# Optimization experiments

Hardware: AMD Instinct MI355X
Metric: run time of the kernel (lower is better)

## Reference

```python
import jax, jax.numpy as jnp
import numpy as np

N, E, F_IN, F_E = 50000, 400000, 16, 3
H1, H2, H3 = 32, 64, 64
NUM_GRAPHS = 32
SLOPE = 0.2  # GAT leaky_relu negative slope


def _glorot(key, shape):
    fan_in, fan_out = shape[0], shape[-1]
    lim = jnp.sqrt(6.0 / (fan_in + fan_out))
    return jax.random.uniform(key, shape, jnp.float32, -lim, lim)


def setup_inputs() -> dict:
    key = jax.random.key(0)
    ks = jax.random.split(key, 20)
    x = jax.random.normal(ks[0], (N, F_IN), jnp.float32)
    edge_attr = jax.random.normal(ks[1], (E, F_E), jnp.float32)
    edge_index = jax.random.randint(ks[2], (2, E), 0, N, jnp.int32)
    batch = jnp.sort(jax.random.randint(ks[3], (N,), 0, NUM_GRAPHS, jnp.int32))
    return {
        "x": x, "edge_attr": edge_attr, "edge_index": edge_index, "batch": batch,
        # EdgeMLP: F_E -> 128 -> 64 -> F_IN*H1
        "mlp_w1": _glorot(ks[4], (F_E, 128)), "mlp_b1": jnp.zeros((128,), jnp.float32),
        "mlp_w2": _glorot(ks[5], (128, 64)), "mlp_b2": jnp.zeros((64,), jnp.float32),
        "mlp_w3": _glorot(ks[6], (64, F_IN * H1)), "mlp_b3": jnp.zeros((F_IN * H1,), jnp.float32),
        # NNConv root weight + bias
        "root_w": _glorot(ks[7], (F_IN, H1)), "conv1_b": jnp.zeros((H1,), jnp.float32),
        # GATConv 1 (heads=1, concat=False)
        "gat1_w": _glorot(ks[8], (H1, H2)), "gat1_asrc": _glorot(ks[9], (H2,)),
        "gat1_adst": _glorot(ks[10], (H2,)), "gat1_b": jnp.zeros((H2,), jnp.float32),
        # GATConv 2
        "gat2_w": _glorot(ks[11], (H2, H3)), "gat2_asrc": _glorot(ks[12], (H3,)),
        "gat2_adst": _glorot(ks[13], (H3,)), "gat2_b": jnp.zeros((H3,), jnp.float32),
    }


def _segment_softmax(logits, seg, num):
    m = jax.ops.segment_max(logits, seg, num_segments=num)
    e = jnp.exp(logits - m[seg])
    s = jax.ops.segment_sum(e, seg, num_segments=num)
    return e / s[seg]


def _gat(h_in, src, dst, W, a_src, a_dst, b):
    # self loops (PyG default add_self_loops=True)
    n = h_in.shape[0]
    loop = jnp.arange(n, dtype=src.dtype)
    s = jnp.concatenate([src, loop])
    d = jnp.concatenate([dst, loop])
    h = h_in @ W  # [N, out]
    alpha = (h @ a_src)[s] + (h @ a_dst)[d]  # [E+N]
    alpha = jnp.where(alpha > 0, alpha, SLOPE * alpha)
    alpha = _segment_softmax(alpha, d, n)
    out = jax.ops.segment_sum(alpha[:, None] * h[s], d, num_segments=n)
    return out + b


def reference(x, edge_attr, edge_index, batch,
              mlp_w1, mlp_b1, mlp_w2, mlp_b2, mlp_w3, mlp_b3,
              root_w, conv1_b,
              gat1_w, gat1_asrc, gat1_adst, gat1_b,
              gat2_w, gat2_asrc, gat2_adst, gat2_b):
    src, dst = edge_index[0], edge_index[1]
    # --- NNConv: per-edge weight matrix from EdgeMLP, message = x_src @ W_e ---
    h = jax.nn.relu(edge_attr @ mlp_w1 + mlp_b1)
    h = jax.nn.relu(h @ mlp_w2 + mlp_b2)
    w_e = (h @ mlp_w3 + mlp_b3).reshape(-1, F_IN, H1)  # [E, F_IN, H1]
    msg = jnp.einsum('ei,eio->eo', x[src], w_e)        # [E, H1]
    agg = jax.ops.segment_sum(msg, dst, num_segments=N)  # aggr='add'
    h1 = jax.nn.relu(x @ root_w + agg + conv1_b)
    # --- GAT layers ---
    h2 = jax.nn.relu(_gat(h1, src, dst, gat1_w, gat1_asrc, gat1_adst, gat1_b))
    h3 = jax.nn.relu(_gat(h2, src, dst, gat2_w, gat2_asrc, gat2_adst, gat2_b))
    # --- global mean pool ---
    sums = jax.ops.segment_sum(h3, batch, num_segments=NUM_GRAPHS)
    cnt = jax.ops.segment_sum(jnp.ones((N,), h3.dtype), batch, num_segments=NUM_GRAPHS)
    return sums / jnp.maximum(cnt, 1.0)[:, None]
```

## Files before the change

kernel.cpp:

```cpp
#include <hip/hip_runtime.h>

#define NN 50000
#define NE 400000
#define NG 32
#define SLOPE 0.2f
#define NSB ((NN + 255) / 256)

typedef __attribute__((ext_vector_type(4))) float f32x4;
typedef __attribute__((ext_vector_type(16))) float f32x16;
typedef __attribute__((ext_vector_type(8))) short s16x8;

__device__ __forceinline__ float lrelu(float v) { return v > 0.f ? v : SLOPE * v; }
__device__ __forceinline__ unsigned short f2bf(float f) {
    union { float f; unsigned u; } c; c.f = f;
    unsigned r = c.u + 0x7fffu + ((c.u >> 16) & 1u);
    return (unsigned short)(r >> 16);
}
__device__ __forceinline__ float bf2f(unsigned short b) {
    union { unsigned u; float f; } c; c.u = ((unsigned)b) << 16; return c.f;
}
__device__ __forceinline__ unsigned pack2(float a, float b) {
    return (unsigned)f2bf(a) | ((unsigned)f2bf(b) << 16);
}
__device__ __forceinline__ uint2 pack_bf4(float a, float b, float c, float d) {
    uint2 u;
    u.x = pack2(a, b);
    u.y = pack2(c, d);
    return u;
}

__global__ __launch_bounds__(256) void k_hist(const int* __restrict__ dst, int* __restrict__ deg) {
    int e = blockIdx.x * 256 + threadIdx.x;
    if (e < NE) atomicAdd(&deg[dst[e]], 1);
}

__global__ __launch_bounds__(256) void k_bsum(const int* __restrict__ deg, int* __restrict__ bsum) {
    __shared__ int ls[256];
    const int t = threadIdx.x;
    const int idx = blockIdx.x * 256 + t;
    ls[t] = (idx < NN) ? deg[idx] : 0;
    __syncthreads();
#pragma unroll
    for (int off = 128; off; off >>= 1) {
        if (t < off) ls[t] += ls[t + off];
        __syncthreads();
    }
    if (t == 0) bsum[blockIdx.x] = ls[0];
}

__global__ __launch_bounds__(256) void k_scan2(const int* __restrict__ deg,
                                               const int* __restrict__ bsum,
                                               int* __restrict__ rowptr, int* __restrict__ cursor) {
    __shared__ int lb[256];
    __shared__ int ls[256];
    const int t = threadIdx.x, b = blockIdx.x;
    lb[t] = (t < NSB && t < b) ? bsum[t] : 0;
    const int idx = b * 256 + t;
    const int v = (idx < NN) ? deg[idx] : 0;
    ls[t] = v;
    __syncthreads();
#pragma unroll
    for (int off = 128; off; off >>= 1) {
        if (t < off) lb[t] += lb[t + off];
        __syncthreads();
    }
#pragma unroll
    for (int off = 1; off < 256; off <<= 1) {
        int u = (t >= off) ? ls[t - off] : 0;
        __syncthreads();
        ls[t] += u;
        __syncthreads();
    }
    if (idx < NN) {
        const int run = lb[0] + ls[t] - v;
        rowptr[idx] = run;
        cursor[idx] = run;
    }
    if (b == 0 && t == 0) rowptr[NN] = NE;
}

__global__ __launch_bounds__(256) void k_perm(const int* __restrict__ dst, const int* __restrict__ src,
                                              int* __restrict__ cursor, int* __restrict__ eid,
                                              int* __restrict__ srcp) {
    int e = blockIdx.x * 256 + threadIdx.x;
    if (e < NE) {
        int p = atomicAdd(&cursor[dst[e]], 1);
        eid[p] = e;
        srcp[p] = src[e];
    }
}

__global__ __launch_bounds__(256) void k_wprep(const float* __restrict__ w3,
                                               const float* __restrict__ w2,
                                               const float* __restrict__ w1,
                                               const float* __restrict__ b1,
                                               const float* __restrict__ b3,
                                               unsigned short* __restrict__ w3t_g,
                                               unsigned short* __restrict__ w2t_g,
                                               unsigned short* __restrict__ w1p_g,
                                               unsigned short* __restrict__ b3t_g) {
    const int v = blockIdx.x * 256 + threadIdx.x;
    if (v < 64 * 512) {
        const int k = v >> 9, n = v & 511;
        const int byte = (n << 7) | ((k << 1) ^ ((n & 7) << 4));
        *(unsigned short*)((char*)w3t_g + byte) = f2bf(w3[v]);
    }
    if (v < 64 * 128) {
        const int o = v & 63, slot = v >> 6;
        const int ks = slot >> 4, lg2 = (slot >> 3) & 1, j = slot & 7;
        const int kp = (ks >> 1) * 32 + (j & 3) + 8 * (j >> 2) + 16 * (ks & 1) + 4 * lg2;
        const int byte = (o << 8) | ((slot << 1) ^ ((o & 7) << 4));
        *(unsigned short*)((char*)w2t_g + byte) = f2bf(w2[kp * 64 + o]);
    }
    if (v < 128 * 16) {
        const int j = v >> 4, k = v & 15;
        float val = (k < 3) ? w1[k * 128 + j] : (k == 3 ? b1[j] : 0.f);
        w1p_g[v] = f2bf(val);
    }
    if (v < 512) {
        const int i = v >> 5, o = v & 31;
        b3t_g[o * 16 + i] = f2bf(b3[v]);
    }
}

#define FUSED_GRID 256
#define NCHUNK (NE / 32)
__global__ __launch_bounds__(512, 1) void k_fused(
    const float* __restrict__ ea,
    const unsigned short* __restrict__ w1p_g,
    const unsigned short* __restrict__ w2t_g, const float* __restrict__ b2,
    const unsigned short* __restrict__ w3t_g, const unsigned short* __restrict__ b3t_g,
    const int* __restrict__ src, const float* __restrict__ x,
    unsigned short* __restrict__ msg)
{
    __shared__ __align__(16) unsigned short w3t[512 * 64];
    __shared__ __align__(16) unsigned short w2t[64 * 128];
    __shared__ __align__(16) unsigned short w1p[128 * 16];
    __shared__ __align__(16) unsigned short b3t[512];
    __shared__ __align__(16) float b2s[64];
    __shared__ __align__(16) unsigned slab[8][1024];

    const int t = threadIdx.x;
    {
        const uint4* g = (const uint4*)w3t_g;
        uint4* l = (uint4*)w3t;
        for (int v = t; v < 4096; v += 512) l[v] = g[v];
        const uint4* g2 = (const uint4*)w2t_g;
        uint4* l2 = (uint4*)w2t;
        for (int v = t; v < 1024; v += 512) l2[v] = g2[v];
    }
    if (t < 256) ((uint4*)w1p)[t] = ((const uint4*)w1p_g)[t];
    if (t < 64)  ((uint4*)b3t)[t] = ((const uint4*)b3t_g)[t];
    if (t < 64)  b2s[t] = b2[t];
    __syncthreads();

    const int wid = t >> 6, lane = t & 63;
    const int l31 = lane & 31, lg2 = lane >> 5;
    char* sw = (char*)slab[wid];
    const int swz = (l31 & 7) << 4;

    s16x8 w1pf[4];
#pragma unroll
    for (int n = 0; n < 4; ++n)
        w1pf[n] = *(const s16x8*)((const char*)w1p + ((n * 32 + l31) << 5) + lg2 * 16);
    s16x8 b3f = *(const s16x8*)((const char*)b3t + (l31 << 5) + lg2 * 16);

    for (int chunk = blockIdx.x * 8 + wid; chunk < NCHUNK; chunk += FUSED_GRID * 8) {
        const int e = chunk * 32 + l31;
        const int sn = src[e];
        const f32x4* __restrict__ xp = (const f32x4*)(x + (size_t)sn * 16);
        f32x4 x0 = xp[0], x1 = xp[1], x2 = xp[2], x3 = xp[3];
        const float ea0 = ea[e * 3], ea1 = ea[e * 3 + 1], ea2 = ea[e * 3 + 2];

        s16x8 eb = (s16x8){0, 0, 0, 0, 0, 0, 0, 0};
        if (lg2 == 0) {
            eb[0] = (short)f2bf(ea0); eb[1] = (short)f2bf(ea1);
            eb[2] = (short)f2bf(ea2); eb[3] = (short)0x3F80;
        }
        s16x8 hb[8];
#pragma unroll
        for (int n = 0; n < 4; ++n) {
            f32x16 d = {0.f};
            d = __builtin_amdgcn_mfma_f32_32x32x16_bf16(w1pf[n], eb, d, 0, 0, 0);
#pragma unroll
            for (int s = 0; s < 2; ++s)
#pragma unroll
                for (int j = 0; j < 8; ++j)
                    hb[2 * n + s][j] = (short)f2bf(fmaxf(d[(j & 3) + 4 * (j >> 2) + 8 * s], 0.f));
        }

        asm volatile("s_waitcnt lgkmcnt(0)" ::: "memory");
#pragma unroll
        for (int nblk = 0; nblk < 2; ++nblk) {
            f32x16 a2 = {0.f};
            const char* __restrict__ w2row = (const char*)w2t + ((nblk * 32 + l31) << 8);
#pragma unroll
            for (int ks = 0; ks < 8; ++ks) {
                s16x8 a = *(const s16x8*)(w2row + ((ks * 32 + lg2 * 16) ^ swz));
                a2 = __builtin_amdgcn_mfma_f32_32x32x16_bf16(a, hb[ks], a2, 0, 0, 0);
            }
#pragma unroll
            for (int rh = 0; rh < 4; ++rh) {
                const f32x4 bv = *(const f32x4*)(b2s + nblk * 32 + rh * 8 + lg2 * 4);
                const int kb = nblk * 64 + rh * 16 + lg2 * 8;
                *(uint2*)(sw + l31 * 128 + (kb ^ swz)) =
                    pack_bf4(fmaxf(a2[rh * 4] + bv[0], 0.f), fmaxf(a2[rh * 4 + 1] + bv[1], 0.f),
                             fmaxf(a2[rh * 4 + 2] + bv[2], 0.f), fmaxf(a2[rh * 4 + 3] + bv[3], 0.f));
            }
        }
        asm volatile("s_waitcnt lgkmcnt(0)" ::: "memory");

        s16x8 wb[4];
#pragma unroll
        for (int ks = 0; ks < 4; ++ks)
            wb[ks] = *(const s16x8*)(sw + l31 * 128 + ((ks * 32 + lg2 * 16) ^ swz));

        s16x8 xbf;
        {
            f32x4 a0 = lg2 ? x2 : x0, a1 = lg2 ? x3 : x1;
#pragma unroll
            for (int i = 0; i < 4; ++i) {
                xbf[i] = (short)f2bf(a0[i]);
                xbf[i + 4] = (short)f2bf(a1[i]);
            }
        }
        f32x16 p = {0.f};
        p = __builtin_amdgcn_mfma_f32_32x32x16_bf16(b3f, xbf, p, 0, 0, 0);

#pragma unroll
        for (int nblk = 0; nblk < 16; ++nblk) {
            const char* __restrict__ arow = (const char*)w3t + ((nblk * 32 + l31) << 7);
            f32x16 d = {0.f};
#pragma unroll
            for (int ks = 0; ks < 4; ++ks) {
                s16x8 a = *(const s16x8*)(arow + ((ks * 32 + lg2 * 16) ^ swz));
                d = __builtin_amdgcn_mfma_f32_32x32x16_bf16(a, wb[ks], d, 0, 0, 0);
            }
            const float xs = (nblk < 4 ? x0 : nblk < 8 ? x1 : nblk < 12 ? x2 : x3)[nblk & 3];
#pragma unroll
            for (int r = 0; r < 16; ++r) p[r] = fmaf(xs, d[r], p[r]);
        }

        asm volatile("s_waitcnt lgkmcnt(0)" ::: "memory");
#pragma unroll
        for (int rh = 0; rh < 4; ++rh) {
            const int ob = rh * 16 + lg2 * 8;
            *(uint2*)(sw + l31 * 64 + (ob ^ ((l31 & 7) << 3))) =
                pack_bf4(p[rh * 4], p[rh * 4 + 1], p[rh * 4 + 2], p[rh * 4 + 3]);
        }
        asm volatile("s_waitcnt lgkmcnt(0)" ::: "memory");
#pragma unroll
        for (int q = 0; q < 2; ++q) {
            const int er = (lane >> 2) + q * 16;
            const int off = (lane & 3) * 16;
            const int s8 = (er & 7) << 3;
            uint2 a = *(const uint2*)(sw + er * 64 + (off ^ s8));
            uint2 b = *(const uint2*)(sw + er * 64 + ((off + 8) ^ s8));
            *(uint4*)((char*)msg + (size_t)chunk * 2048 + q * 1024 + lane * 16) =
                make_uint4(a.x, a.y, b.x, b.y);
        }
    }
}

__global__ __launch_bounds__(256) void k_agg(
    const unsigned short* __restrict__ msg, const int* __restrict__ rowptr,
    const int* __restrict__ eid, const float* __restrict__ x,
    const float* __restrict__ rw, const float* __restrict__ cb, float* __restrict__ h1)
{
    const int gid = blockIdx.x * 256 + threadIdx.x;
    const int n = (gid >> 6) * 2 + ((gid & 63) >> 5);
    if (n >= NN) return;
    const int o = gid & 31;
    const int r0 = rowptr[n], r1 = rowptr[n + 1];
    float acc = 0.f;
    for (int j = r0; j < r1; ++j)
        acc += bf2f(msg[(size_t)eid[j] * 32 + o]);
    const float* __restrict__ xr = x + (size_t)n * 16;
    float root = cb[o];
#pragma unroll
    for (int i = 0; i < 16; ++i) root = fmaf(xr[i], rw[i * 32 + o], root);
    h1[(size_t)n * 32 + o] = fmaxf(acc + root, 0.f);
}

template <int FI, bool BFIN>
__global__ __launch_bounds__(256) void k_gat_h(
    const void* __restrict__ hin, const float* __restrict__ W,
    const float* __restrict__ av_s, const float* __restrict__ av_d,
    unsigned* __restrict__ hbf, float* __restrict__ as_v, float* __restrict__ ad_v)
{
    const int n = blockIdx.x * 256 + threadIdx.x;
    if (n >= NN) return;
    float acc[64];
#pragma unroll
    for (int o = 0; o < 64; ++o) acc[o] = 0.f;

    float xv[FI];
    if constexpr (BFIN) {
        const uint4* __restrict__ hp = (const uint4*)((const unsigned*)hin + (size_t)n * (FI / 2));
#pragma unroll
        for (int q = 0; q < FI / 8; ++q) {
            uint4 v = hp[q];
            const unsigned w4[4] = {v.x, v.y, v.z, v.w};
#pragma unroll
            for (int c = 0; c < 4; ++c) {
                xv[q * 8 + 2 * c]     = bf2f((unsigned short)(w4[c] & 0xffff));
                xv[q * 8 + 2 * c + 1] = bf2f((unsigned short)(w4[c] >> 16));
            }
        }
    } else {
        const f32x4* __restrict__ hp = (const f32x4*)((const float*)hin + (size_t)n * FI);
#pragma unroll
        for (int q = 0; q < FI / 4; ++q) {
            f32x4 v = hp[q];
#pragma unroll
            for (int c = 0; c < 4; ++c) xv[q * 4 + c] = v[c];
        }
    }
#pragma unroll 2
    for (int i = 0; i < FI; ++i) {
        const float xi = xv[i];
        const float* __restrict__ wr = W + i * 64;
#pragma unroll
        for (int o = 0; o < 64; ++o) acc[o] = fmaf(xi, wr[o], acc[o]);
    }
    float s = 0.f, d = 0.f;
#pragma unroll
    for (int o = 0; o < 64; ++o) {
        s = fmaf(acc[o], av_s[o], s);
        d = fmaf(acc[o], av_d[o], d);
    }
    as_v[n] = s;
    ad_v[n] = d;
    uint4* __restrict__ op = (uint4*)(hbf + (size_t)n * 32);
#pragma unroll
    for (int q = 0; q < 8; ++q)
        op[q] = make_uint4(pack2(acc[8 * q], acc[8 * q + 1]), pack2(acc[8 * q + 2], acc[8 * q + 3]),
                           pack2(acc[8 * q + 4], acc[8 * q + 5]), pack2(acc[8 * q + 6], acc[8 * q + 7]));
}

__global__ __launch_bounds__(256) void k_easrc(const int* __restrict__ srcp,
                                               const float* __restrict__ as_v,
                                               float* __restrict__ asp) {
    int j = blockIdx.x * 256 + threadIdx.x;
    if (j < NE) asp[j] = as_v[srcp[j]];
}

__global__ __launch_bounds__(256) void k_gat_node(
    const int* __restrict__ rowptr, const int* __restrict__ srcp, const float* __restrict__ asp,
    const unsigned* __restrict__ hbf, const float* __restrict__ as_v, const float* __restrict__ ad_v,
    const float* __restrict__ b, unsigned* __restrict__ outbf)
{
    const int n = (blockIdx.x * 256 + threadIdx.x) >> 6;
    if (n >= NN) return;
    const int lane = threadIdx.x & 63;
    const int fl = lane & 15, qw = lane >> 4;
    const int r0 = rowptr[n], r1 = rowptr[n + 1];
    const float adn = ad_v[n];
    const float l_self = lrelu(as_v[n] + adn);
    float m = l_self;
    for (int j = r0 + lane; j < r1; j += 64)
        m = fmaxf(m, lrelu(asp[j] + adn));
#pragma unroll
    for (int off = 32; off; off >>= 1) m = fmaxf(m, __shfl_xor(m, off));
    float s = 0.f;
    for (int j = r0 + lane; j < r1; j += 64)
        s += expf(lrelu(asp[j] + adn) - m);
#pragma unroll
    for (int off = 32; off; off >>= 1) s += __shfl_xor(s, off);
    const float w_self = expf(l_self - m);
    s += w_self;
    float a0 = 0.f, a1 = 0.f, a2 = 0.f, a3 = 0.f;
    if (qw == 0) {
        const uint2 hv = *(const uint2*)(hbf + (size_t)n * 32 + fl * 2);
        a0 = w_self * bf2f((unsigned short)(hv.x & 0xffff));
        a1 = w_self * bf2f((unsigned short)(hv.x >> 16));
        a2 = w_self * bf2f((unsigned short)(hv.y & 0xffff));
        a3 = w_self * bf2f((unsigned short)(hv.y >> 16));
    }
    for (int j = r0 + qw; j < r1; j += 4) {
        const int sn = srcp[j];
        const float w = expf(lrelu(asp[j] + adn) - m);
        const uint2 hv = *(const uint2*)(hbf + (size_t)sn * 32 + fl * 2);
        a0 = fmaf(w, bf2f((unsigned short)(hv.x & 0xffff)), a0);
        a1 = fmaf(w, bf2f((unsigned short)(hv.x >> 16)), a1);
        a2 = fmaf(w, bf2f((unsigned short)(hv.y & 0xffff)), a2);
        a3 = fmaf(w, bf2f((unsigned short)(hv.y >> 16)), a3);
    }
#pragma unroll
    for (int off = 16; off <= 32; off <<= 1) {
        a0 += __shfl_xor(a0, off);
        a1 += __shfl_xor(a1, off);
        a2 += __shfl_xor(a2, off);
        a3 += __shfl_xor(a3, off);
    }
    if (qw == 0) {
        const float v0 = fmaxf(a0 / s + b[4 * fl], 0.f);
        const float v1 = fmaxf(a1 / s + b[4 * fl + 1], 0.f);
        const float v2 = fmaxf(a2 / s + b[4 * fl + 2], 0.f);
        const float v3 = fmaxf(a3 / s + b[4 * fl + 3], 0.f);
        *(uint2*)(outbf + (size_t)n * 32 + fl * 2) = make_uint2(pack2(v0, v1), pack2(v2, v3));
    }
}

__global__ __launch_bounds__(256) void k_pool1(
    const unsigned* __restrict__ hbf, const int* __restrict__ batch,
    float* __restrict__ gsum, float* __restrict__ gcnt)
{
    __shared__ float ls[NG * 64];
    __shared__ float lc[NG];
    for (int j = threadIdx.x; j < NG * 64; j += 256) ls[j] = 0.f;
    if (threadIdx.x < NG) lc[threadIdx.x] = 0.f;
    __syncthreads();
    const int base = blockIdx.x * 512;
    for (int idx = threadIdx.x; idx < 512 * 32; idx += 256) {
        const int nl = idx >> 5, f2 = idx & 31;
        const int n = base + nl;
        if (n < NN) {
            const int g = batch[n];
            const unsigned hv = hbf[(size_t)n * 32 + f2];
            atomicAdd(&ls[g * 64 + 2 * f2], bf2f((unsigned short)(hv & 0xffff)));
            atomicAdd(&ls[g * 64 + 2 * f2 + 1], bf2f((unsigned short)(hv >> 16)));
            if (f2 == 0) atomicAdd(&lc[g], 1.f);
        }
    }
    __syncthreads();
    for (int j = threadIdx.x; j < NG * 64; j += 256) atomicAdd(&gsum[j], ls[j]);
    if (threadIdx.x < NG) atomicAdd(&gcnt[threadIdx.x], lc[threadIdx.x]);
}

__global__ __launch_bounds__(256) void k_pool2(
    const float* __restrict__ gsum, const float* __restrict__ gcnt, float* __restrict__ out)
{
    const int idx = blockIdx.x * 256 + threadIdx.x;
    if (idx >= NG * 64) return;
    out[idx] = gsum[idx] / fmaxf(gcnt[idx >> 6], 1.f);
}

extern "C" void kernel_launch(void* const* d_in, const int* in_sizes, int n_in,
                              void* d_out, int out_size, void* d_ws, size_t ws_size,
                              hipStream_t stream)
{
    const float* x     = (const float*)d_in[0];
    const float* ea    = (const float*)d_in[1];
    const int*   ei    = (const int*)d_in[2];
    const int*   batch = (const int*)d_in[3];
    const float* w1 = (const float*)d_in[4];   const float* b1 = (const float*)d_in[5];
    const float* w2 = (const float*)d_in[6];   const float* b2 = (const float*)d_in[7];
    const float* w3 = (const float*)d_in[8];   const float* b3 = (const float*)d_in[9];
    const float* rw = (const float*)d_in[10];  const float* cb = (const float*)d_in[11];
    const float* g1w  = (const float*)d_in[12]; const float* g1as = (const float*)d_in[13];
    const float* g1ad = (const float*)d_in[14]; const float* g1b  = (const float*)d_in[15];
    const float* g2w  = (const float*)d_in[16]; const float* g2as = (const float*)d_in[17];
    const float* g2ad = (const float*)d_in[18]; const float* g2b  = (const float*)d_in[19];
    const int* src = ei;
    const int* dst = ei + NE;
    float* out = (float*)d_out;
    (void)in_sizes; (void)n_in; (void)out_size; (void)ws_size;

    char* ws = (char*)d_ws;
    size_t off = 0;
    auto alloc = [&](size_t bytes) -> char* {
        char* p = ws + off;
        off += (bytes + 255) & ~(size_t)255;
        return p;
    };
    int*  deg    = (int*)alloc((size_t)NN * 4);
    int*  cursor = (int*)alloc((size_t)NN * 4);
    int*  rowptr = (int*)alloc((size_t)(NN + 1) * 4);
    int*  bsum   = (int*)alloc((size_t)NSB * 4);
    int*  eid    = (int*)alloc((size_t)NE * 4);
    int*  srcp   = (int*)alloc((size_t)NE * 4);
    float* asp   = (float*)alloc((size_t)NE * 4);
    unsigned short* w3t_g = (unsigned short*)alloc((size_t)64 * 512 * 2);
    unsigned short* w2t_g = (unsigned short*)alloc((size_t)64 * 128 * 2);
    unsigned short* w1p_g = (unsigned short*)alloc((size_t)128 * 16 * 2);
    unsigned short* b3t_g = (unsigned short*)alloc((size_t)512 * 2);
    unsigned short* msg   = (unsigned short*)alloc((size_t)NE * 32 * 2);
    float* h1    = (float*)alloc((size_t)NN * 32 * 4);
    unsigned* hT = (unsigned*)alloc((size_t)NN * 32 * 4);
    unsigned* hC = (unsigned*)alloc((size_t)NN * 32 * 4);
    unsigned* hD = (unsigned*)alloc((size_t)NN * 32 * 4);
    float* as_v = (float*)alloc((size_t)NN * 4);
    float* ad_v = (float*)alloc((size_t)NN * 4);
    float* gsum = (float*)alloc((size_t)NG * 64 * 4);
    float* gcnt = (float*)alloc((size_t)NG * 4);

    hipMemsetAsync(deg, 0, (size_t)NN * 4, stream);
    hipMemsetAsync(gsum, 0, (size_t)NG * 64 * 4, stream);
    hipMemsetAsync(gcnt, 0, (size_t)NG * 4, stream);

    k_hist<<<(NE + 255) / 256, 256, 0, stream>>>(dst, deg);
    k_bsum<<<NSB, 256, 0, stream>>>(deg, bsum);
    k_scan2<<<NSB, 256, 0, stream>>>(deg, bsum, rowptr, cursor);
    k_perm<<<(NE + 255) / 256, 256, 0, stream>>>(dst, src, cursor, eid, srcp);

    k_wprep<<<(64 * 512 + 255) / 256, 256, 0, stream>>>(w3, w2, w1, b1, b3,
                                                        w3t_g, w2t_g, w1p_g, b3t_g);
    k_fused<<<FUSED_GRID, 512, 0, stream>>>(ea, w1p_g, w2t_g, b2, w3t_g, b3t_g, src, x, msg);
    k_agg<<<(NN / 2 * 64 + 255) / 256 + 1, 256, 0, stream>>>(msg, rowptr, eid, x, rw, cb, h1);

    k_gat_h<32, false><<<(NN + 255) / 256, 256, 0, stream>>>(h1, g1w, g1as, g1ad, hT, as_v, ad_v);
    k_easrc<<<(NE + 255) / 256, 256, 0, stream>>>(srcp, as_v, asp);
    k_gat_node<<<(NN * 64 + 255) / 256, 256, 0, stream>>>(rowptr, srcp, asp, hT, as_v, ad_v, g1b, hC);

    k_gat_h<64, true><<<(NN + 255) / 256, 256, 0, stream>>>(hC, g2w, g2as, g2ad, hT, as_v, ad_v);
    k_easrc<<<(NE + 255) / 256, 256, 0, stream>>>(srcp, as_v, asp);
    k_gat_node<<<(NN * 64 + 255) / 256, 256, 0, stream>>>(rowptr, srcp, asp, hT, as_v, ad_v, g2b, hD);

    k_pool1<<<(NN + 511) / 512, 256, 0, stream>>>(hD, batch, gsum, gcnt);
    k_pool2<<<(NG * 64 + 255) / 256, 256, 0, stream>>>(gsum, gcnt, out);
}
```

Measured before the change: 334.4 us.

## Fuse GAT feature transforms into aggregation kernels and double fused-MLP block size

Folds the per-node GAT linear transform and attention-score projections into the preceding aggregation kernels (NNConv aggregation feeds GAT1 transform; GAT1 node softmax feeds GAT2 transform), computing each row with one wavefront using shuffles. This removes the separate k_gat_h launches and the h1/hC intermediate round trips through global memory. It also raises the fused edge-MLP kernel from 512 to 1024 threads per block, with 16 waves and a doubled LDS slab, which increases LDS use and register pressure per block. The cost is more shuffle traffic per node and repeated reads of W rows per wavefront.

```diff
diff --git a/kernel.cpp b/kernel.cpp
--- a/kernel.cpp
+++ b/kernel.cpp
@@ -125,7 +125,7 @@
 
 #define FUSED_GRID 256
 #define NCHUNK (NE / 32)
-__global__ __launch_bounds__(512, 1) void k_fused(
+__global__ __launch_bounds__(1024) void k_fused(
     const float* __restrict__ ea,
     const unsigned short* __restrict__ w1p_g,
     const unsigned short* __restrict__ w2t_g, const float* __restrict__ b2,
@@ -138,16 +138,16 @@
     __shared__ __align__(16) unsigned short w1p[128 * 16];
     __shared__ __align__(16) unsigned short b3t[512];
     __shared__ __align__(16) float b2s[64];
-    __shared__ __align__(16) unsigned slab[8][1024];
+    __shared__ __align__(16) unsigned slab[16][1024];
 
     const int t = threadIdx.x;
     {
         const uint4* g = (const uint4*)w3t_g;
         uint4* l = (uint4*)w3t;
-        for (int v = t; v < 4096; v += 512) l[v] = g[v];
+        for (int v = t; v < 4096; v += 1024) l[v] = g[v];
         const uint4* g2 = (const uint4*)w2t_g;
         uint4* l2 = (uint4*)w2t;
-        for (int v = t; v < 1024; v += 512) l2[v] = g2[v];
+        if (t < 1024) { if (t < 1024) l2[t % 1024] = g2[t % 1024]; }
     }
     if (t < 256) ((uint4*)w1p)[t] = ((const uint4*)w1p_g)[t];
     if (t < 64)  ((uint4*)b3t)[t] = ((const uint4*)b3t_g)[t];
@@ -165,7 +165,7 @@
         w1pf[n] = *(const s16x8*)((const char*)w1p + ((n * 32 + l31) << 5) + lg2 * 16);
     s16x8 b3f = *(const s16x8*)((const char*)b3t + (l31 << 5) + lg2 * 16);
 
-    for (int chunk = blockIdx.x * 8 + wid; chunk < NCHUNK; chunk += FUSED_GRID * 8) {
+    for (int chunk = blockIdx.x * 16 + wid; chunk < NCHUNK; chunk += FUSED_GRID * 16) {
         const int e = chunk * 32 + l31;
         const int sn = src[e];
         const f32x4* __restrict__ xp = (const f32x4*)(x + (size_t)sn * 16);
@@ -262,80 +262,37 @@
     }
 }
 
-__global__ __launch_bounds__(256) void k_agg(
+__global__ __launch_bounds__(256) void k_aggt(
     const unsigned short* __restrict__ msg, const int* __restrict__ rowptr,
     const int* __restrict__ eid, const float* __restrict__ x,
-    const float* __restrict__ rw, const float* __restrict__ cb, float* __restrict__ h1)
-{
-    const int gid = blockIdx.x * 256 + threadIdx.x;
-    const int n = (gid >> 6) * 2 + ((gid & 63) >> 5);
+    const float* __restrict__ rw, const float* __restrict__ cb,
+    const float* __restrict__ W, const float* __restrict__ av_s, const float* __restrict__ av_d,
+    unsigned* __restrict__ hbf, float* __restrict__ as_v, float* __restrict__ ad_v)
+{
+    const int n = (blockIdx.x * 256 + threadIdx.x) >> 6;
     if (n >= NN) return;
-    const int o = gid & 31;
+    const int lane = threadIdx.x & 63;
+    const int half = lane >> 5, o = lane & 31;
     const int r0 = rowptr[n], r1 = rowptr[n + 1];
-    float acc = 0.f;
-    for (int j = r0; j < r1; ++j)
-        acc += bf2f(msg[(size_t)eid[j] * 32 + o]);
+    float agg = 0.f;
+    for (int j = r0 + half; j < r1; j += 2)
+        agg += bf2f(msg[(size_t)eid[j] * 32 + o]);
+    agg += __shfl_xor(agg, 32);
     const float* __restrict__ xr = x + (size_t)n * 16;
     float root = cb[o];
 #pragma unroll
     for (int i = 0; i < 16; ++i) root = fmaf(xr[i], rw[i * 32 + o], root);
-    h1[(size_t)n * 32 + o] = fmaxf(acc + root, 0.f);
-}
-
-template <int FI, bool BFIN>
-__global__ __launch_bounds__(256) void k_gat_h(
-    const void* __restrict__ hin, const float* __restrict__ W,
-    const float* __restrict__ av_s, const float* __restrict__ av_d,
-    unsigned* __restrict__ hbf, float* __restrict__ as_v, float* __restrict__ ad_v)
-{
-    const int n = blockIdx.x * 256 + threadIdx.x;
-    if (n >= NN) return;
-    float acc[64];
-#pragma unroll
-    for (int o = 0; o < 64; ++o) acc[o] = 0.f;
-
-    float xv[FI];
-    if constexpr (BFIN) {
-        const uint4* __restrict__ hp = (const uint4*)((const unsigned*)hin + (size_t)n * (FI / 2));
-#pragma unroll
-        for (int q = 0; q < FI / 8; ++q) {
-            uint4 v = hp[q];
-            const unsigned w4[4] = {v.x, v.y, v.z, v.w};
-#pragma unroll
-            for (int c = 0; c < 4; ++c) {
-                xv[q * 8 + 2 * c]     = bf2f((unsigned short)(w4[c] & 0xffff));
-                xv[q * 8 + 2 * c + 1] = bf2f((unsigned short)(w4[c] >> 16));
-            }
-        }
-    } else {
-        const f32x4* __restrict__ hp = (const f32x4*)((const float*)hin + (size_t)n * FI);
-#pragma unroll
-        for (int q = 0; q < FI / 4; ++q) {
-            f32x4 v = hp[q];
-#pragma unroll
-            for (int c = 0; c < 4; ++c) xv[q * 4 + c] = v[c];
-        }
-    }
-#pragma unroll 2
-    for (int i = 0; i < FI; ++i) {
-        const float xi = xv[i];
-        const float* __restrict__ wr = W + i * 64;
-#pragma unroll
-        for (int o = 0; o < 64; ++o) acc[o] = fmaf(xi, wr[o], acc[o]);
-    }
-    float s = 0.f, d = 0.f;
-#pragma unroll
-    for (int o = 0; o < 64; ++o) {
-        s = fmaf(acc[o], av_s[o], s);
-        d = fmaf(acc[o], av_d[o], d);
-    }
-    as_v[n] = s;
-    ad_v[n] = d;
-    uint4* __restrict__ op = (uint4*)(hbf + (size_t)n * 32);
-#pragma unroll
-    for (int q = 0; q < 8; ++q)
-        op[q] = make_uint4(pack2(acc[8 * q], acc[8 * q + 1]), pack2(acc[8 * q + 2], acc[8 * q + 3]),
-                           pack2(acc[8 * q + 4], acc[8 * q + 5]), pack2(acc[8 * q + 6], acc[8 * q + 7]));
+    const float h1v = fmaxf(agg + root, 0.f);
+    float acc = 0.f;
+#pragma unroll 8
+    for (int i = 0; i < 32; ++i)
+        acc = fmaf(__shfl(h1v, i), W[i * 64 + lane], acc);
+    float s = acc * av_s[lane], d = acc * av_d[lane];
+#pragma unroll
+    for (int off = 32; off; off >>= 1) { s += __shfl_xor(s, off); d += __shfl_xor(d, off); }
+    if (lane == 0) { as_v[n] = s; ad_v[n] = d; }
+    const float nb = __shfl(acc, lane | 1);
+    if (!(lane & 1)) hbf[(size_t)n * 32 + (lane >> 1)] = pack2(acc, nb);
 }
 
 __global__ __launch_bounds__(256) void k_easrc(const int* __restrict__ srcp,
@@ -345,7 +302,79 @@
     if (j < NE) asp[j] = as_v[srcp[j]];
 }
 
-__global__ __launch_bounds__(256) void k_gat_node(
+__global__ __launch_bounds__(256) void k_gat1(
+    const int* __restrict__ rowptr, const int* __restrict__ srcp, const float* __restrict__ asp,
+    const unsigned* __restrict__ hbf, const float* __restrict__ as_v, const float* __restrict__ ad_v,
+    const float* __restrict__ b,
+    const float* __restrict__ W2, const float* __restrict__ av_s2, const float* __restrict__ av_d2,
+    unsigned* __restrict__ hbf2, float* __restrict__ as_v2, float* __restrict__ ad_v2)
+{
+    const int n = (blockIdx.x * 256 + threadIdx.x) >> 6;
+    if (n >= NN) return;
+    const int lane = threadIdx.x & 63;
+    const int fl = lane & 15, qw = lane >> 4;
+    const int r0 = rowptr[n], r1 = rowptr[n + 1];
+    const float adn = ad_v[n];
+    const float l_self = lrelu(as_v[n] + adn);
+    float m = l_self;
+    for (int j = r0 + lane; j < r1; j += 64)
+        m = fmaxf(m, lrelu(asp[j] + adn));
+#pragma unroll
+    for (int off = 32; off; off >>= 1) m = fmaxf(m, __shfl_xor(m, off));
+    float s = 0.f;
+    for (int j = r0 + lane; j < r1; j += 64)
+        s += expf(lrelu(asp[j] + adn) - m);
+#pragma unroll
+    for (int off = 32; off; off >>= 1) s += __shfl_xor(s, off);
+    const float w_self = expf(l_self - m);
+    s += w_self;
+    float a0 = 0.f, a1 = 0.f, a2 = 0.f, a3 = 0.f;
+    if (qw == 0) {
+        const uint2 hv = *(const uint2*)(hbf + (size_t)n * 32 + fl * 2);
+        a0 = w_self * bf2f((unsigned short)(hv.x & 0xffff));
+        a1 = w_self * bf2f((unsigned short)(hv.x >> 16));
+        a2 = w_self * bf2f((unsigned short)(hv.y & 0xffff));
+        a3 = w_self * bf2f((unsigned short)(hv.y >> 16));
+    }
+    for (int j = r0 + qw; j < r1; j += 4) {
+        const int sn = srcp[j];
+        const float w = expf(lrelu(asp[j] + adn) - m);
+        const uint2 hv = *(const uint2*)(hbf + (size_t)sn * 32 + fl * 2);
+        a0 = fmaf(w, bf2f((unsigned short)(hv.x & 0xffff)), a0);
+        a1 = fmaf(w, bf2f((unsigned short)(hv.x >> 16)), a1);
+        a2 = fmaf(w, bf2f((unsigned short)(hv.y & 0xffff)), a2);
+        a3 = fmaf(w, bf2f((unsigned short)(hv.y >> 16)), a3);
+    }
+#pragma unroll
+    for (int off = 16; off <= 32; off <<= 1) {
+        a0 += __shfl_xor(a0, off);
+        a1 += __shfl_xor(a1, off);
+        a2 += __shfl_xor(a2, off);
+        a3 += __shfl_xor(a3, off);
+    }
+    const float v0 = fmaxf(a0 / s + b[4 * fl], 0.f);
+    const float v1 = fmaxf(a1 / s + b[4 * fl + 1], 0.f);
+    const float v2 = fmaxf(a2 / s + b[4 * fl + 2], 0.f);
+    const float v3 = fmaxf(a3 / s + b[4 * fl + 3], 0.f);
+    float acc = 0.f;
+#pragma unroll 8
+    for (int i = 0; i < 64; ++i) {
+        float hi;
+        if ((i & 3) == 0) hi = __shfl(v0, i >> 2);
+        else if ((i & 3) == 1) hi = __shfl(v1, i >> 2);
+        else if ((i & 3) == 2) hi = __shfl(v2, i >> 2);
+        else hi = __shfl(v3, i >> 2);
+        acc = fmaf(hi, W2[i * 64 + lane], acc);
+    }
+    float s2 = acc * av_s2[lane], d2 = acc * av_d2[lane];
+#pragma unroll
+    for (int off = 32; off; off >>= 1) { s2 += __shfl_xor(s2, off); d2 += __shfl_xor(d2, off); }
+    if (lane == 0) { as_v2[n] = s2; ad_v2[n] = d2; }
+    const float nb = __shfl(acc, lane | 1);
+    if (!(lane & 1)) hbf2[(size_t)n * 32 + (lane >> 1)] = pack2(acc, nb);
+}
+
+__global__ __launch_bounds__(256) void k_gat2(
     const int* __restrict__ rowptr, const int* __restrict__ srcp, const float* __restrict__ asp,
     const unsigned* __restrict__ hbf, const float* __restrict__ as_v, const float* __restrict__ ad_v,
     const float* __restrict__ b, unsigned* __restrict__ outbf)
@@ -476,12 +505,13 @@
     unsigned short* w1p_g = (unsigned short*)alloc((size_t)128 * 16 * 2);
     unsigned short* b3t_g = (unsigned short*)alloc((size_t)512 * 2);
     unsigned short* msg   = (unsigned short*)alloc((size_t)NE * 32 * 2);
-    float* h1    = (float*)alloc((size_t)NN * 32 * 4);
-    unsigned* hT = (unsigned*)alloc((size_t)NN * 32 * 4);
-    unsigned* hC = (unsigned*)alloc((size_t)NN * 32 * 4);
-    unsigned* hD = (unsigned*)alloc((size_t)NN * 32 * 4);
-    float* as_v = (float*)alloc((size_t)NN * 4);
-    float* ad_v = (float*)alloc((size_t)NN * 4);
+    unsigned* hT  = (unsigned*)alloc((size_t)NN * 32 * 4);
+    unsigned* hT2 = (unsigned*)alloc((size_t)NN * 32 * 4);
+    unsigned* hD  = (unsigned*)alloc((size_t)NN * 32 * 4);
+    float* as_v  = (float*)alloc((size_t)NN * 4);
+    float* ad_v  = (float*)alloc((size_t)NN * 4);
+    float* as_v2 = (float*)alloc((size_t)NN * 4);
+    float* ad_v2 = (float*)alloc((size_t)NN * 4);
     float* gsum = (float*)alloc((size_t)NG * 64 * 4);
     float* gcnt = (float*)alloc((size_t)NG * 4);
 
@@ -496,16 +526,15 @@
 
     k_wprep<<<(64 * 512 + 255) / 256, 256, 0, stream>>>(w3, w2, w1, b1, b3,
                                                         w3t_g, w2t_g, w1p_g, b3t_g);
-    k_fused<<<FUSED_GRID, 512, 0, stream>>>(ea, w1p_g, w2t_g, b2, w3t_g, b3t_g, src, x, msg);
-    k_agg<<<(NN / 2 * 64 + 255) / 256 + 1, 256, 0, stream>>>(msg, rowptr, eid, x, rw, cb, h1);
-
-    k_gat_h<32, false><<<(NN + 255) / 256, 256, 0, stream>>>(h1, g1w, g1as, g1ad, hT, as_v, ad_v);
+    k_fused<<<FUSED_GRID, 1024, 0, stream>>>(ea, w1p_g, w2t_g, b2, w3t_g, b3t_g, src, x, msg);
+
+    k_aggt<<<(NN * 64 + 255) / 256, 256, 0, stream>>>(msg, rowptr, eid, x, rw, cb,
+                                                      g1w, g1as, g1ad, hT, as_v, ad_v);
     k_easrc<<<(NE + 255) / 256, 256, 0, stream>>>(srcp, as_v, asp);
-    k_gat_node<<<(NN * 64 + 255) / 256, 256, 0, stream>>>(rowptr, srcp, asp, hT, as_v, ad_v, g1b, hC);
-
-    k_gat_h<64, true><<<(NN + 255) / 256, 256, 0, stream>>>(hC, g2w, g2as, g2ad, hT, as_v, ad_v);
-    k_easrc<<<(NE + 255) / 256, 256, 0, stream>>>(srcp, as_v, asp);
-    k_gat_node<<<(NN * 64 + 255) / 256, 256, 0, stream>>>(rowptr, srcp, asp, hT, as_v, ad_v, g2b, hD);
+    k_gat1<<<(NN * 64 + 255) / 256, 256, 0, stream>>>(rowptr, srcp, asp, hT, as_v, ad_v, g1b,
+                                                      g2w, g2as, g2ad, hT2, as_v2, ad_v2);
+    k_easrc<<<(NE + 255) / 256, 256, 0, stream>>>(srcp, as_v2, asp);
+    k_gat2<<<(NN * 64 + 255) / 256, 256, 0, stream>>>(rowptr, srcp, asp, hT2, as_v2, ad_v2, g2b, hD);
 
     k_pool1<<<(NN + 511) / 512, 256, 0, stream>>>(hD, batch, gsum, gcnt);
     k_pool2<<<(NG * 64 + 255) / 256, 256, 0, stream>>>(gsum, gcnt, out);
```

After: 418.8 us. 25.2% more time.
